# Kernel optimization log

Hardware: AMD Instinct MI355X
Metric: run time of the kernel (lower is better)

## Reference

```python
import jax, jax.numpy as jnp
import numpy as np

S, D_MODEL, D_RNN = 256, 512, 512  # module's broadcasting requires d_rnn == d_model


def setup_inputs() -> dict:
    key = jax.random.key(0)
    k1, k2, k3, k4 = jax.random.split(key, 4)
    x = jax.random.normal(k1, (S, D_MODEL), dtype=jnp.float32)
    state = jnp.zeros((D_RNN, D_MODEL), dtype=jnp.float32)
    # equinox nn.Linear default init: U[-1/sqrt(in), 1/sqrt(in)] for weight and bias
    lim = 1.0 / np.sqrt(D_MODEL)
    W1 = jax.random.uniform(k2, (2 * D_RNN, D_MODEL), minval=-lim, maxval=lim, dtype=jnp.float32)
    b1 = jax.random.uniform(k3, (2 * D_RNN,), minval=-lim, maxval=lim, dtype=jnp.float32)
    # Lambda init exactly as in source: inv_sigmoid(p) = log(1/(1-p)), bounds ** (1/8)
    inv_sig = lambda p: np.log(1.0 / (1.0 - p))
    lower = float(np.power(inv_sig(0.9), 1.0 / 8.0))
    upper = float(np.power(inv_sig(0.999), 1.0 / 8.0))
    Lambda = jax.random.uniform(k4, (D_MODEL,), minval=lower, maxval=upper, dtype=jnp.float32)
    return {"x": x, "state": state, "W1": W1, "b1": b1, "Lambda": Lambda}


def reference(x, state, W1, b1, Lambda):
    # lin1 applied per timestep: (S, d_model) @ (d_model, 2*d_rnn)
    z = jax.nn.sigmoid(x @ W1.T + b1)              # (S, 2*d_rnn)
    inp, rec = jnp.split(z, 2, axis=-1)            # each (S, d_rnn)
    # recurrence gate a_t in (0,1): exp(-8 * softplus(Lambda) * rec)
    a = jnp.exp(-8.0 * jax.nn.softplus(Lambda)[None, :] * rec)  # (S, d_rnn)
    # gated input: outer product per step -> (S, d_rnn, d_model)
    gated_x = jnp.einsum('is,is,id->isd', jnp.sqrt(1.0 - a * a), inp, x)

    def step(h, xs):
        g, at = xs
        h = at[:, None] * h + g                    # (d_rnn, d_model)
        return h, h

    state, y = jax.lax.scan(step, state, (gated_x, a))
    return (y, state)
```

## Files before the change

### kernel.cpp

```cpp
#include <hip/hip_runtime.h>
#include <hip/hip_bf16.h>

#define S_LEN 256
#define DM    512
#define DR    512

typedef float f4 __attribute__((ext_vector_type(4)));
typedef float f2 __attribute__((ext_vector_type(2)));


__global__ __launch_bounds__(256) void k_transpose_x(const float* __restrict__ x,
                                                     float* __restrict__ xT) {
    __shared__ float tile[32][33];
    const int k0 = blockIdx.x * 32;
    const int t0 = blockIdx.y * 32;
    const int lx = threadIdx.x & 31;
    const int ly = threadIdx.x >> 5;
#pragma unroll
    for (int i = 0; i < 32; i += 8)
        tile[ly + i][lx] = x[(t0 + ly + i) * DM + k0 + lx];
    __syncthreads();
#pragma unroll
    for (int i = 0; i < 32; i += 8)
        xT[(k0 + ly + i) * S_LEN + t0 + lx] = tile[lx][ly + i];
}

__global__ __launch_bounds__(256) void k_gemm(const float* __restrict__ xT,
                                              const float* __restrict__ W1,
                                              float* __restrict__ part) {
    const int bx = blockIdx.x;
    const int sp = bx >> 3;
    const int ke = bx & 7;
    const int t  = threadIdx.x;

    const int r0 = 2 * sp, r1 = 2 * sp + 1;
    const int r2 = DR + 2 * sp, r3 = DR + 2 * sp + 1;

    const f4* __restrict__ W0 = reinterpret_cast<const f4*>(W1 + r0 * DM + ke * 64);
    const f4* __restrict__ Wp = reinterpret_cast<const f4*>(W1 + r1 * DM + ke * 64);
    const f4* __restrict__ W2 = reinterpret_cast<const f4*>(W1 + r2 * DM + ke * 64);
    const f4* __restrict__ W3 = reinterpret_cast<const f4*>(W1 + r3 * DM + ke * 64);
    const float* __restrict__ xb = xT + (ke * 64) * S_LEN + t;

    float a0 = 0.f, a1 = 0.f, a2 = 0.f, a3 = 0.f;

#pragma unroll 4
    for (int kk = 0; kk < 16; ++kk) {
        const float x0 = xb[(4 * kk + 0) * S_LEN];
        const float x1 = xb[(4 * kk + 1) * S_LEN];
        const float x2 = xb[(4 * kk + 2) * S_LEN];
        const float x3 = xb[(4 * kk + 3) * S_LEN];
        const f4 w0 = W0[kk];
        const f4 w1 = Wp[kk];
        const f4 w2 = W2[kk];
        const f4 w3 = W3[kk];
        a0 = fmaf(x0, w0.x, a0); a0 = fmaf(x1, w0.y, a0);
        a0 = fmaf(x2, w0.z, a0); a0 = fmaf(x3, w0.w, a0);
        a1 = fmaf(x0, w1.x, a1); a1 = fmaf(x1, w1.y, a1);
        a1 = fmaf(x2, w1.z, a1); a1 = fmaf(x3, w1.w, a1);
        a2 = fmaf(x0, w2.x, a2); a2 = fmaf(x1, w2.y, a2);
        a2 = fmaf(x2, w2.z, a2); a2 = fmaf(x3, w2.w, a2);
        a3 = fmaf(x0, w3.x, a3); a3 = fmaf(x1, w3.y, a3);
        a3 = fmaf(x2, w3.z, a3); a3 = fmaf(x3, w3.w, a3);
    }

    float* __restrict__ pb = part + ke * (1024 * 256);
    pb[r0 * 256 + t] = a0;
    pb[r1 * 256 + t] = a1;
    pb[r2 * 256 + t] = a2;
    pb[r3 * 256 + t] = a3;
}

__global__ __launch_bounds__(256) void k_rec(const float* __restrict__ x,
                                             const float* __restrict__ state0,
                                             const float* __restrict__ part,
                                             const float* __restrict__ b1,
                                             const float* __restrict__ Lam,
                                             f4* __restrict__ out4) {
    const int bx   = blockIdx.x;
    const int sp   = (bx & 7) * 32 + (bx >> 3);
    const int tid  = threadIdx.x;
    const int half = tid >> 7;
    const int s    = sp * 2 + half;
    const int dq   = tid & 127;

    __shared__ f2 ac_l[2][S_LEN];

    const int P = 1024 * 256;
#pragma unroll
    for (int sl = 0; sl < 2; ++sl) {
        const int srow = sp * 2 + sl;
        const int tt   = tid;
        if (tt < S_LEN) {
            float pi = b1[srow];
            float pr = b1[DR + srow];
#pragma unroll
            for (int e = 0; e < 8; ++e) {
                pi += part[e * P + srow * 256 + tt];
                pr += part[e * P + (DR + srow) * 256 + tt];
            }
            const float inp = 1.f / (1.f + expf(-pi));
            const float rec = 1.f / (1.f + expf(-pr));
            const float sof = log1pf(expf(Lam[srow]));
            const float a   = expf(-8.f * sof * rec);
            const float c   = sqrtf(fmaxf(1.f - a * a, 0.f)) * inp;
            f2 ac; ac.x = a; ac.y = c;
            ac_l[sl][tt] = ac;
        }
    }

    const f4* __restrict__ st4 = reinterpret_cast<const f4*>(state0);
    f4 h = st4[s * 128 + dq];

    const f4* __restrict__ x4 = reinterpret_cast<const f4*>(x);
    f4 xv = x4[dq];

    __syncthreads();

#pragma unroll 4
    for (int t = 0; t < S_LEN; ++t) {
        f4 xn;
        if (t + 1 < S_LEN) xn = x4[(t + 1) * 128 + dq];
        else xn = (f4)0.f;

        const f2 ac = ac_l[half][t];
        const float at = ac.x, ct = ac.y;
        h.x = fmaf(at, h.x, ct * xv.x);
        h.y = fmaf(at, h.y, ct * xv.y);
        h.z = fmaf(at, h.z, ct * xv.z);
        h.w = fmaf(at, h.w, ct * xv.w);

        __builtin_nontemporal_store(h, &out4[(t * DR + s) * 128 + dq]);
        xv = xn;
    }
    out4[(S_LEN * DR) * 128 + s * 128 + dq] = h;
}

extern "C" void kernel_launch(void* const* d_in, const int* in_sizes, int n_in,
                              void* d_out, int out_size, void* d_ws, size_t ws_size,
                              hipStream_t stream) {
    const float* x      = (const float*)d_in[0];
    const float* state0 = (const float*)d_in[1];
    const float* W1     = (const float*)d_in[2];
    const float* b1     = (const float*)d_in[3];
    const float* Lam    = (const float*)d_in[4];

    float* ws   = (float*)d_ws;
    float* xT   = ws;
    float* part = ws + 131072;

    f4* out4 = (f4*)d_out;

    k_transpose_x<<<dim3(16, 8), 256, 0, stream>>>(x, xT);
    k_gemm<<<dim3(2048), 256, 0, stream>>>(xT, W1, part);
    k_rec<<<dim3(256), 256, 0, stream>>>(x, state0, part, b1, Lam, out4);
}
```

Before: 63.82 us.

## Pack transposed x as float4 and compute eight weight rows per GEMM block

The transpose kernel now writes x in a k-packed float4 layout, so each GEMM thread fetches four k values with one vector load instead of four scalar loads. Each GEMM block now computes eight output rows instead of four, which halves the grid and reuses each x load across more weight rows. The gate-precompute loop in the recurrence kernel drops a redundant bounds check. Runtime is likely dominated by the recurrence kernel's output writes, so the GEMM changes may matter little, and the extra accumulators raise register use.

```diff
diff --git a/kernel.cpp b/kernel.cpp
--- a/kernel.cpp
+++ b/kernel.cpp
@@ -10,7 +10,7 @@
 
 
 __global__ __launch_bounds__(256) void k_transpose_x(const float* __restrict__ x,
-                                                     float* __restrict__ xT) {
+                                                     f4* __restrict__ xP) {
     __shared__ float tile[32][33];
     const int k0 = blockIdx.x * 32;
     const int t0 = blockIdx.y * 32;
@@ -20,55 +20,74 @@
     for (int i = 0; i < 32; i += 8)
         tile[ly + i][lx] = x[(t0 + ly + i) * DM + k0 + lx];
     __syncthreads();
-#pragma unroll
-    for (int i = 0; i < 32; i += 8)
-        xT[(k0 + ly + i) * S_LEN + t0 + lx] = tile[lx][ly + i];
+    f4 v;
+    v.x = tile[lx][4 * ly + 0];
+    v.y = tile[lx][4 * ly + 1];
+    v.z = tile[lx][4 * ly + 2];
+    v.w = tile[lx][4 * ly + 3];
+    xP[(k0 / 4 + ly) * S_LEN + t0 + lx] = v;
 }
 
-__global__ __launch_bounds__(256) void k_gemm(const float* __restrict__ xT,
+__global__ __launch_bounds__(256) void k_gemm(const f4* __restrict__ xP,
                                               const float* __restrict__ W1,
                                               float* __restrict__ part) {
     const int bx = blockIdx.x;
-    const int sp = bx >> 3;
+    const int sq = bx >> 3;
     const int ke = bx & 7;
     const int t  = threadIdx.x;
 
-    const int r0 = 2 * sp, r1 = 2 * sp + 1;
-    const int r2 = DR + 2 * sp, r3 = DR + 2 * sp + 1;
+    const f4* __restrict__ W0 = reinterpret_cast<const f4*>(W1 + (4 * sq + 0) * DM + ke * 64);
+    const f4* __restrict__ Wa = reinterpret_cast<const f4*>(W1 + (4 * sq + 1) * DM + ke * 64);
+    const f4* __restrict__ Wb = reinterpret_cast<const f4*>(W1 + (4 * sq + 2) * DM + ke * 64);
+    const f4* __restrict__ Wc = reinterpret_cast<const f4*>(W1 + (4 * sq + 3) * DM + ke * 64);
+    const f4* __restrict__ W4 = reinterpret_cast<const f4*>(W1 + (DR + 4 * sq + 0) * DM + ke * 64);
+    const f4* __restrict__ W5 = reinterpret_cast<const f4*>(W1 + (DR + 4 * sq + 1) * DM + ke * 64);
+    const f4* __restrict__ W6 = reinterpret_cast<const f4*>(W1 + (DR + 4 * sq + 2) * DM + ke * 64);
+    const f4* __restrict__ W7 = reinterpret_cast<const f4*>(W1 + (DR + 4 * sq + 3) * DM + ke * 64);
 
-    const f4* __restrict__ W0 = reinterpret_cast<const f4*>(W1 + r0 * DM + ke * 64);
-    const f4* __restrict__ Wp = reinterpret_cast<const f4*>(W1 + r1 * DM + ke * 64);
-    const f4* __restrict__ W2 = reinterpret_cast<const f4*>(W1 + r2 * DM + ke * 64);
-    const f4* __restrict__ W3 = reinterpret_cast<const f4*>(W1 + r3 * DM + ke * 64);
-    const float* __restrict__ xb = xT + (ke * 64) * S_LEN + t;
+    const f4* __restrict__ xb = xP + (ke * 16) * S_LEN + t;
 
     float a0 = 0.f, a1 = 0.f, a2 = 0.f, a3 = 0.f;
+    float a4 = 0.f, a5 = 0.f, a6 = 0.f, a7 = 0.f;
 
 #pragma unroll 4
     for (int kk = 0; kk < 16; ++kk) {
-        const float x0 = xb[(4 * kk + 0) * S_LEN];
-        const float x1 = xb[(4 * kk + 1) * S_LEN];
-        const float x2 = xb[(4 * kk + 2) * S_LEN];
-        const float x3 = xb[(4 * kk + 3) * S_LEN];
+        const f4 xv = xb[kk * S_LEN];
         const f4 w0 = W0[kk];
-        const f4 w1 = Wp[kk];
-        const f4 w2 = W2[kk];
-        const f4 w3 = W3[kk];
-        a0 = fmaf(x0, w0.x, a0); a0 = fmaf(x1, w0.y, a0);
-        a0 = fmaf(x2, w0.z, a0); a0 = fmaf(x3, w0.w, a0);
-        a1 = fmaf(x0, w1.x, a1); a1 = fmaf(x1, w1.y, a1);
-        a1 = fmaf(x2, w1.z, a1); a1 = fmaf(x3, w1.w, a1);
-        a2 = fmaf(x0, w2.x, a2); a2 = fmaf(x1, w2.y, a2);
-        a2 = fmaf(x2, w2.z, a2); a2 = fmaf(x3, w2.w, a2);
-        a3 = fmaf(x0, w3.x, a3); a3 = fmaf(x1, w3.y, a3);
-        a3 = fmaf(x2, w3.z, a3); a3 = fmaf(x3, w3.w, a3);
+        const f4 w1 = Wa[kk];
+        const f4 w2 = Wb[kk];
+        const f4 w3 = Wc[kk];
+        const f4 w4 = W4[kk];
+        const f4 w5 = W5[kk];
+        const f4 w6 = W6[kk];
+        const f4 w7 = W7[kk];
+        a0 = fmaf(xv.x, w0.x, a0); a0 = fmaf(xv.y, w0.y, a0);
+        a0 = fmaf(xv.z, w0.z, a0); a0 = fmaf(xv.w, w0.w, a0);
+        a1 = fmaf(xv.x, w1.x, a1); a1 = fmaf(xv.y, w1.y, a1);
+        a1 = fmaf(xv.z, w1.z, a1); a1 = fmaf(xv.w, w1.w, a1);
+        a2 = fmaf(xv.x, w2.x, a2); a2 = fmaf(xv.y, w2.y, a2);
+        a2 = fmaf(xv.z, w2.z, a2); a2 = fmaf(xv.w, w2.w, a2);
+        a3 = fmaf(xv.x, w3.x, a3); a3 = fmaf(xv.y, w3.y, a3);
+        a3 = fmaf(xv.z, w3.z, a3); a3 = fmaf(xv.w, w3.w, a3);
+        a4 = fmaf(xv.x, w4.x, a4); a4 = fmaf(xv.y, w4.y, a4);
+        a4 = fmaf(xv.z, w4.z, a4); a4 = fmaf(xv.w, w4.w, a4);
+        a5 = fmaf(xv.x, w5.x, a5); a5 = fmaf(xv.y, w5.y, a5);
+        a5 = fmaf(xv.z, w5.z, a5); a5 = fmaf(xv.w, w5.w, a5);
+        a6 = fmaf(xv.x, w6.x, a6); a6 = fmaf(xv.y, w6.y, a6);
+        a6 = fmaf(xv.z, w6.z, a6); a6 = fmaf(xv.w, w6.w, a6);
+        a7 = fmaf(xv.x, w7.x, a7); a7 = fmaf(xv.y, w7.y, a7);
+        a7 = fmaf(xv.z, w7.z, a7); a7 = fmaf(xv.w, w7.w, a7);
     }
 
     float* __restrict__ pb = part + ke * (1024 * 256);
-    pb[r0 * 256 + t] = a0;
-    pb[r1 * 256 + t] = a1;
-    pb[r2 * 256 + t] = a2;
-    pb[r3 * 256 + t] = a3;
+    pb[(4 * sq + 0) * 256 + t] = a0;
+    pb[(4 * sq + 1) * 256 + t] = a1;
+    pb[(4 * sq + 2) * 256 + t] = a2;
+    pb[(4 * sq + 3) * 256 + t] = a3;
+    pb[(DR + 4 * sq + 0) * 256 + t] = a4;
+    pb[(DR + 4 * sq + 1) * 256 + t] = a5;
+    pb[(DR + 4 * sq + 2) * 256 + t] = a6;
+    pb[(DR + 4 * sq + 3) * 256 + t] = a7;
 }
 
 __global__ __launch_bounds__(256) void k_rec(const float* __restrict__ x,
@@ -90,23 +109,20 @@
 #pragma unroll
     for (int sl = 0; sl < 2; ++sl) {
         const int srow = sp * 2 + sl;
-        const int tt   = tid;
-        if (tt < S_LEN) {
-            float pi = b1[srow];
-            float pr = b1[DR + srow];
+        float pi = b1[srow];
+        float pr = b1[DR + srow];
 #pragma unroll
-            for (int e = 0; e < 8; ++e) {
-                pi += part[e * P + srow * 256 + tt];
-                pr += part[e * P + (DR + srow) * 256 + tt];
-            }
-            const float inp = 1.f / (1.f + expf(-pi));
-            const float rec = 1.f / (1.f + expf(-pr));
-            const float sof = log1pf(expf(Lam[srow]));
-            const float a   = expf(-8.f * sof * rec);
-            const float c   = sqrtf(fmaxf(1.f - a * a, 0.f)) * inp;
-            f2 ac; ac.x = a; ac.y = c;
-            ac_l[sl][tt] = ac;
+        for (int e = 0; e < 8; ++e) {
+            pi += part[e * P + srow * 256 + tid];
+            pr += part[e * P + (DR + srow) * 256 + tid];
         }
+        const float inp = 1.f / (1.f + expf(-pi));
+        const float rec = 1.f / (1.f + expf(-pr));
+        const float sof = log1pf(expf(Lam[srow]));
+        const float a   = expf(-8.f * sof * rec);
+        const float c   = sqrtf(fmaxf(1.f - a * a, 0.f)) * inp;
+        f2 ac; ac.x = a; ac.y = c;
+        ac_l[sl][tid] = ac;
     }
 
     const f4* __restrict__ st4 = reinterpret_cast<const f4*>(state0);
@@ -146,12 +162,12 @@
     const float* Lam    = (const float*)d_in[4];
 
     float* ws   = (float*)d_ws;
-    float* xT   = ws;
+    f4*    xP   = (f4*)ws;
     float* part = ws + 131072;
 
     f4* out4 = (f4*)d_out;
 
-    k_transpose_x<<<dim3(16, 8), 256, 0, stream>>>(x, xT);
-    k_gemm<<<dim3(2048), 256, 0, stream>>>(xT, W1, part);
+    k_transpose_x<<<dim3(16, 8), 256, 0, stream>>>(x, xP);
+    k_gemm<<<dim3(1024), 256, 0, stream>>>(xP, W1, part);
     k_rec<<<dim3(256), 256, 0, stream>>>(x, state0, part, b1, Lam, out4);
 }
```

Result: slower. 66.17 us (+3.7%).
